# Optimization experiments

Measured on AMD Instinct MI355X. Metric: run time of the kernel, lower is better.

The kernel has to match this reference:

```python
import jax, jax.numpy as jnp
import numpy as np
from jax import lax

PART = 224   # PART_IMAGE_SIZE
PAD = 224    # PAD_SIZE
TOPN = 4
IOU_THRESH = 0.25
N_ANCHORS = 1614


def _conv(x, w, b, stride, pad):
    y = lax.conv_general_dilated(x, w, (stride, stride), [(pad, pad), (pad, pad)],
                                 dimension_numbers=('NCHW', 'OIHW', 'NCHW'))
    return y + b[None, :, None, None]


def _iou(box, boxes):
    # box [4], boxes [N,4] as (y0,x0,y1,x1)
    yy0 = jnp.maximum(box[0], boxes[:, 0]); xx0 = jnp.maximum(box[1], boxes[:, 1])
    yy1 = jnp.minimum(box[2], boxes[:, 2]); xx1 = jnp.minimum(box[3], boxes[:, 3])
    inter = jnp.clip(yy1 - yy0, 0.0) * jnp.clip(xx1 - xx0, 0.0)
    a = (box[2] - box[0]) * (box[3] - box[1])
    areas = (boxes[:, 2] - boxes[:, 0]) * (boxes[:, 3] - boxes[:, 1])
    return inter / (a + areas - inter)


def _nms(scores, boxes):
    # hard NMS keeping TOPN boxes; returns indices [TOPN]
    valid = jnp.ones(scores.shape, dtype=bool)
    idxs = []
    for _ in range(TOPN):
        i = jnp.argmax(jnp.where(valid, scores, -jnp.inf))
        idxs.append(i)
        valid = valid & (_iou(boxes[i], boxes) <= IOU_THRESH)
    return jnp.stack(idxs)


def _crop_resize(img, box):
    # img [3,Hp,Wp] padded image, box [4] float; bilinear, align_corners=True,
    # matching F.interpolate(x_pad[:, :, y0:y1, x0:x1], (PART, PART))
    Hp, Wp = img.shape[1], img.shape[2]
    def coords(c0, c1, L):
        t = jnp.arange(PART, dtype=img.dtype) / (PART - 1)
        c = c0 + (c1 - 1.0 - c0) * t          # absolute source coordinate
        cf = jnp.floor(c)
        lo = jnp.clip(cf.astype(jnp.int32), 0, L - 1)
        hi = jnp.clip(lo + 1, 0, L - 1)
        return lo, hi, c - cf
    yl, yh, wy = coords(box[0], box[2], Hp)
    xl, xh, wx = coords(box[1], box[3], Wp)
    g = lambda yi, xi: img[:, yi[:, None], xi[None, :]]   # [3,PART,PART]
    return ((1 - wy)[:, None] * ((1 - wx) * g(yl, xl) + wx * g(yl, xh))
            + wy[:, None] * ((1 - wx) * g(yh, xl) + wx * g(yh, xh)))


def setup_inputs() -> dict:
    key = jax.random.key(0)
    ks = jax.random.split(key, 20)
    x = jax.random.uniform(ks[0], (16, 3, 448, 448), dtype=jnp.float32)
    rpn_feature = jax.random.normal(ks[1], (16, 2048, 14, 14), dtype=jnp.float32)
    # valid boxes inside the padded 896x896 image
    y0 = jax.random.randint(ks[2], (N_ANCHORS,), 0, 560)
    x0 = jax.random.randint(ks[3], (N_ANCHORS,), 0, 560)
    h = jax.random.randint(ks[4], (N_ANCHORS,), 32, 336)
    w = jax.random.randint(ks[5], (N_ANCHORS,), 32, 336)
    anchors = jnp.stack([y0, x0, jnp.minimum(y0 + h, 896), jnp.minimum(x0 + w, 896)], axis=1).astype(jnp.int32)
    s = 0.02
    inp = {
        'x': x, 'rpn_feature': rpn_feature, 'anchors': anchors,
        'w_down1': jax.random.normal(ks[6], (128, 2048, 3, 3), jnp.float32) * s,
        'b_down1': jnp.zeros((128,), jnp.float32),
        'w_down2': jax.random.normal(ks[7], (128, 128, 3, 3), jnp.float32) * s,
        'b_down2': jnp.zeros((128,), jnp.float32),
        'w_down3': jax.random.normal(ks[8], (128, 128, 3, 3), jnp.float32) * s,
        'b_down3': jnp.zeros((128,), jnp.float32),
        'w_tidy1': jax.random.normal(ks[9], (6, 128, 1, 1), jnp.float32) * s,
        'b_tidy1': jnp.zeros((6,), jnp.float32),
        'w_tidy2': jax.random.normal(ks[10], (6, 128, 1, 1), jnp.float32) * s,
        'b_tidy2': jnp.zeros((6,), jnp.float32),
        'w_tidy3': jax.random.normal(ks[11], (9, 128, 1, 1), jnp.float32) * s,
        'b_tidy3': jnp.zeros((9,), jnp.float32),
    }
    return inp


def reference(x, rpn_feature, anchors,
              w_down1, b_down1, w_down2, b_down2, w_down3, b_down3,
              w_tidy1, b_tidy1, w_tidy2, b_tidy2, w_tidy3, b_tidy3):
    B = x.shape[0]
    # ProposalNet
    d1 = jax.nn.relu(_conv(rpn_feature, w_down1, b_down1, 1, 1))   # [B,128,14,14]
    d2 = jax.nn.relu(_conv(d1, w_down2, b_down2, 2, 1))            # [B,128,7,7]
    d3 = jax.nn.relu(_conv(d2, w_down3, b_down3, 2, 1))            # [B,128,4,4]
    t1 = _conv(d1, w_tidy1, b_tidy1, 1, 0).reshape(B, -1)
    t2 = _conv(d2, w_tidy2, b_tidy2, 1, 0).reshape(B, -1)
    t3 = _conv(d3, w_tidy3, b_tidy3, 1, 0).reshape(B, -1)
    rpn_score = jnp.concatenate([t1, t2, t3], axis=1)              # [B, 1614]
    boxes = anchors.astype(x.dtype)                                # [N,4]
    top_n_index = jax.vmap(lambda s: _nms(s, boxes))(rpn_score)    # [B,TOPN]
    top_n_prob = jnp.take_along_axis(rpn_score, top_n_index, axis=1)
    x_pad = jnp.pad(x, ((0, 0), (0, 0), (PAD, PAD), (PAD, PAD)))   # [B,3,896,896]
    sel_boxes = boxes[top_n_index]                                 # [B,TOPN,4]
    part_imgs = jax.vmap(lambda img, bxs: jax.vmap(lambda b: _crop_resize(img, b))(bxs))(x_pad, sel_boxes)
    # part_imgs: [B,TOPN,3,PART,PART]
    return rpn_score, top_n_index, top_n_prob, part_imgs
```

## Files before the change

### kernel.cpp

```cpp
#include <hip/hip_runtime.h>
#include <hip/hip_bf16.h>

#define NB 16
#define NA 1614
#define NBP (NB * 196 * 128)

typedef __bf16 bf16x8 __attribute__((ext_vector_type(8)));
typedef float f32x4 __attribute__((ext_vector_type(4)));

__device__ __forceinline__ unsigned short f2bf(float v) {
  unsigned u = __float_as_uint(v);
  unsigned r = (u + 0x7FFFu + ((u >> 16) & 1u)) >> 16;
  return (unsigned short)r;
}
__device__ __forceinline__ float bf2f(unsigned short s) {
  return __uint_as_float(((unsigned)s) << 16);
}

__global__ __launch_bounds__(256)
void prep(const float* __restrict__ w, const float* __restrict__ in,
          unsigned short* __restrict__ wTh, unsigned short* __restrict__ wTl,
          unsigned short* __restrict__ aTh, unsigned short* __restrict__ aTl) {
  __shared__ float s[32 * 201];
  const int bid = blockIdx.x;
  if (bid < 1024) {
    const int chunk = bid & 63, b = bid >> 6;
    const float* src = in + ((size_t)b * 2048 + chunk * 32) * 196;
#pragma unroll
    for (int r = 0; r < 7; r++) {
      int e = threadIdx.x + 256 * r;
      if (e < 1568) {
        int ic = e / 49, f = e - ic * 49;
        float4 v = ((const float4*)(src + (size_t)ic * 196))[f];
        float* d = s + ic * 201 + f * 4;
        d[0] = v.x; d[1] = v.y; d[2] = v.z; d[3] = v.w;
      }
    }
    __syncthreads();
    unsigned short* oh = aTh + (size_t)bid * (196 * 32);
    unsigned short* ol = aTl + (size_t)bid * (196 * 32);
#pragma unroll
    for (int r = 0; r < 4; r++) {
      int e = threadIdx.x + 256 * r;
      if (e < 784) {
        int pos = e >> 2, part = e & 3;
        unsigned short hv[8], lv[8];
#pragma unroll
        for (int j = 0; j < 8; j++) {
          float v = s[(part * 8 + j) * 201 + pos];
          unsigned short h = f2bf(v);
          hv[j] = h;
          lv[j] = f2bf(v - bf2f(h));
        }
        ((uint4*)oh)[e] = *(uint4*)hv;
        ((uint4*)ol)[e] = *(uint4*)lv;
      }
    }
  } else {
    int e = (bid - 1024) * 256 + threadIdx.x;
    if (e < 9 * 128 * 2048) {
      int tap = e / (128 * 2048);
      int rem = e - tap * (128 * 2048);
      int oc = rem >> 11, ic = rem & 2047;
      int kcp = ic >> 7, ks = (ic >> 5) & 3, icq = (ic >> 3) & 3, j = ic & 7;
      size_t g2 = ((size_t)(kcp * 36 + tap * 4 + ks) << 12) + oc * 32 + icq * 8 + j;
      float v = w[((size_t)oc * 2048 + ic) * 9 + tap];
      unsigned short h = f2bf(v);
      wTh[g2] = h;
      wTl[g2] = f2bf(v - bf2f(h));
    }
  }
}

#define APL 1360
#define ABUF (4 * APL)

#define LOADB(H, L, T, K)                                                     \
  {                                                                           \
    const size_t o_ = ((size_t)(kc * 36 + (T) * 4 + (K)) << 12) + bln;        \
    const unsigned short* ph_ = wTh + o_;                                     \
    const unsigned short* pq_ = wTl + o_;                                     \
    H[0] = *(const bf16x8*)(ph_);                                             \
    H[1] = *(const bf16x8*)(ph_ + 512);                                       \
    L[0] = *(const bf16x8*)(pq_);                                             \
    L[1] = *(const bf16x8*)(pq_ + 512);                                       \
  }

#define STEP(IT, BUH, BUL, BNH, BNL)                                          \
  {                                                                           \
    const int it_ = (IT);                                                     \
    const int ks_ = it_ / 9, tap_ = it_ - ks_ * 9;                            \
    {             \
      const int ni_ = (it_ < 35) ? it_ + 1 : 35;                              \
      const int nk_ = ni_ / 9, nt_ = ni_ - nk_ * 9;                           \
      LOADB(BNH, BNL, nt_, nk_);                                              \
    }                                                                         \
    if (ks_ < 3) {        \
      if (tap_ == 3 || tap_ == 4) {                                           \
        int e_ = tid + 256 * (tap_ - 3);                                      \
        if (e_ < ne) {                                                        \
          int u_ = pos04 + e_;                                                \
          int pos_ = u_ >> 2, part_ = u_ & 3;                                 \
          int py_ = pos_ / 14, px_ = pos_ - py_ * 14;                         \
          int d_ = (((ks_ + 1) & 1) ? ABUF : 0) + part_ * APL                 \
                   + (py_ + 1 - rowoff) * 136 + (px_ + 1) * 8;                \
          *(uint4*)(sAh + d_) = sgh;                                          \
          *(uint4*)(sAl + d_) = sgl;                                          \
        }                                                                     \
      }                                                                       \
      if (tap_ == 2 || tap_ == 3) {                                           \
        const uint4* gh_ = (const uint4*)(aTh + ((size_t)(b * 64 + kc * 4 + ks_ + 1) * 196) * 32); \
        const uint4* gl_ = (const uint4*)(aTl + ((size_t)(b * 64 + kc * 4 + ks_ + 1) * 196) * 32); \
        int e_ = tid + 256 * (tap_ - 2);                                      \
        if (e_ < ne) { sgh = gh_[pos04 + e_]; sgl = gl_[pos04 + e_]; }        \
      }                                                                       \
    }                                                                         \
    const int t8_ = (tap_ / 3) * 136 + (tap_ - (tap_ / 3) * 3) * 8;           \
    const unsigned short* pah_ = sAh + (ks_ & 1) * ABUF + qoff + t8_;         \
    const unsigned short* pal_ = sAl + (ks_ & 1) * ABUF + qoff + t8_;         \
    bf16x8 afh[7], afl[7];                                                    \
    _Pragma("unroll") for (int mf = 0; mf < 7; mf++) {                        \
      afh[mf] = *(const bf16x8*)(pah_ + abase[mf]);                           \
      afl[mf] = *(const bf16x8*)(pal_ + abase[mf]);                           \
    }                                                                         \
    _Pragma("unroll") for (int mf = 0; mf < 7; mf++)                          \
      _Pragma("unroll") for (int nf = 0; nf < 2; nf++)                        \
        acc[mf][nf] = __builtin_amdgcn_mfma_f32_16x16x32_bf16(afh[mf], BUH[nf], acc[mf][nf], 0, 0, 0); \
    _Pragma("unroll") for (int mf = 0; mf < 7; mf++)                          \
      _Pragma("unroll") for (int nf = 0; nf < 2; nf++)                        \
        acc[mf][nf] = __builtin_amdgcn_mfma_f32_16x16x32_bf16(afl[mf], BUH[nf], acc[mf][nf], 0, 0, 0); \
    _Pragma("unroll") for (int mf = 0; mf < 7; mf++)                          \
      _Pragma("unroll") for (int nf = 0; nf < 2; nf++)                        \
        acc[mf][nf] = __builtin_amdgcn_mfma_f32_16x16x32_bf16(afh[mf], BUL[nf], acc[mf][nf], 0, 0, 0); \
    if (tap_ == 8) __syncthreads();                                           \
  }

__global__ __launch_bounds__(256, 2)
void conv1_mfma(const unsigned short* __restrict__ aTh, const unsigned short* __restrict__ aTl,
                const unsigned short* __restrict__ wTh, const unsigned short* __restrict__ wTl,
                float* __restrict__ p1) {
  const int bid = blockIdx.x;
  const int kc = bid & 15;
  const int b  = (bid >> 4) & 15;
  const int mh = bid >> 8;
  const int tid = threadIdx.x;
  const int wid = tid >> 6, lane = tid & 63;
  const int wn = wid;
  const int q = lane >> 4, ln = lane & 15;

  __shared__ unsigned short sAh[2 * ABUF];
  __shared__ unsigned short sAl[2 * ABUF];

  const int rowoff = 6 * mh;
  const int pos0 = mh ? 98 : 0;
  const int ne   = mh ? 392 : 504;
  const int pos04 = pos0 * 4;

  for (int e = tid; e < 2 * ABUF / 2; e += 256) {
    ((unsigned int*)sAh)[e] = 0u;
    ((unsigned int*)sAl)[e] = 0u;
  }

  int abase[7];
#pragma unroll
  for (int mf = 0; mf < 7; mf++) {
    int row = mh * 112 + mf * 16 + ln;
    int y = row / 14, x = row - y * 14;
    abase[mf] = (row < 196) ? ((y - rowoff) * 136 + x * 8) : 0;
  }
  const int qoff = q * APL;
  const int bln = (wn * 32 + ln) * 32 + q * 8;

  f32x4 acc[7][2];
#pragma unroll
  for (int mf = 0; mf < 7; mf++)
#pragma unroll
    for (int nf = 0; nf < 2; nf++) acc[mf][nf] = (f32x4){0.f, 0.f, 0.f, 0.f};

  uint4 sgh = {}, sgl = {};

  __syncthreads();

  {
    const uint4* gh = (const uint4*)(aTh + ((size_t)(b * 64 + kc * 4) * 196) * 32);
    const uint4* gl = (const uint4*)(aTl + ((size_t)(b * 64 + kc * 4) * 196) * 32);
#pragma unroll
    for (int r = 0; r < 2; r++) {
      int e = tid + 256 * r;
      if (e < ne) {
        int u = pos04 + e;
        int pos = u >> 2, part = u & 3;
        int py = pos / 14, px = pos - py * 14;
        int d = part * APL + (py + 1 - rowoff) * 136 + (px + 1) * 8;
        *(uint4*)(sAh + d) = gh[u];
        *(uint4*)(sAl + d) = gl[u];
      }
    }
  }
  bf16x8 b0h[2], b0l[2], b1h[2], b1l[2];
  LOADB(b0h, b0l, 0, 0);
  __syncthreads();

  for (int it = 0; it < 36; it += 2) {
    STEP(it,     b0h, b0l, b1h, b1l);
    STEP(it + 1, b1h, b1l, b0h, b0l);
  }

  float* pk = p1 + ((size_t)kc * NB + b) * 196 * 128;
#pragma unroll
  for (int mf = 0; mf < 7; mf++) {
    const int row0 = mh * 112 + mf * 16 + q * 4;
#pragma unroll
    for (int nf = 0; nf < 2; nf++) {
      const int oc = wn * 32 + nf * 16 + ln;
#pragma unroll
      for (int r = 0; r < 4; r++) {
        const int row = row0 + r;
        if (row < 196) pk[(size_t)row * 128 + oc] = acc[mf][nf][r];
      }
    }
  }
}

__global__ __launch_bounds__(256)
void conv1_finish_p(const float* __restrict__ p1, const float* __restrict__ bias,
                    float* __restrict__ d1) {
  __shared__ float s[28 * 132];
  const int bid = blockIdx.x;
  const int pt = bid % 7, b = bid / 7;
  const int tid = threadIdx.x;
#pragma unroll
  for (int r = 0; r < 4; r++) {
    int u = tid + 256 * r;
    if (u < 896) {
      int pos = u >> 5, oc4 = u & 31;
      const float* base = p1 + ((size_t)(b * 196 + pt * 28 + pos)) * 128 + oc4 * 4;
      float4 sum = ((const float4*)bias)[oc4];
#pragma unroll
      for (int k = 0; k < 16; k++) {
        float4 v = *(const float4*)(base + (size_t)k * NBP);
        sum.x += v.x; sum.y += v.y; sum.z += v.z; sum.w += v.w;
      }
      sum.x = fmaxf(sum.x, 0.f); sum.y = fmaxf(sum.y, 0.f);
      sum.z = fmaxf(sum.z, 0.f); sum.w = fmaxf(sum.w, 0.f);
      *(float4*)(s + pos * 132 + oc4 * 4) = sum;
    }
  }
  __syncthreads();
#pragma unroll
  for (int r = 0; r < 4; r++) {
    int u = tid + 256 * r;
    if (u < 896) {
      int oc = u / 7, f = u - oc * 7;
      float4 v;
      v.x = s[(f * 4 + 0) * 132 + oc];
      v.y = s[(f * 4 + 1) * 132 + oc];
      v.z = s[(f * 4 + 2) * 132 + oc];
      v.w = s[(f * 4 + 3) * 132 + oc];
      *(float4*)(d1 + ((size_t)b * 128 + oc) * 196 + pt * 28 + f * 4) = v;
    }
  }
}

__global__ void conv2_part(const float* __restrict__ d1, const float* __restrict__ w,
                           float* __restrict__ p2) {
  const int bid = blockIdx.x;
  const int kc = bid & 3, oct = (bid >> 2) & 3, b = bid >> 4;
  const int ic0 = kc * 32, oc0 = oct * 32;
  const int tid = threadIdx.x;
  const int ocl = tid >> 3, rw = tid & 7;

  __shared__ float s_in[32 * 320];
  __shared__ float s_w[32 * 324];

#pragma unroll
  for (int r = 0; r < 32; r++) {
    const int e = tid + 256 * r;
    const int ch = e >> 8, idx = e & 255;
    const int tr = idx >> 4, tc = idx & 15;
    const int iy = tr - 1, ix = tc - 1;
    float v = 0.f;
    if ((unsigned)iy < 14u && (unsigned)ix < 14u)
      v = d1[((size_t)b * 128 + ic0 + ch) * 196 + iy * 14 + ix];
    s_in[ch * 320 + tr * 20 + tc] = v;
  }
#pragma unroll
  for (int r = 0; r < 36; r++) {
    const int e = tid + 256 * r;
    const int oc = e / 288, rem = e - oc * 288;
    const int ch = rem / 9, tap = rem - ch * 9;
    s_w[ch * 324 + tap * 36 + oc] =
        w[(size_t)(oc0 + oc) * 1152 + (size_t)ic0 * 9 + rem];
  }
  __syncthreads();

  if (rw < 7) {
    float acc[7] = {};
    for (int ic = 0; ic < 32; ic++) {
      const float* wrow = s_w + ic * 324 + ocl;
      const float* irow = s_in + ic * 320;
#pragma unroll
      for (int ky = 0; ky < 3; ky++) {
        const float* r = irow + (2 * rw + ky) * 20;
        const float4 f0 = *(const float4*)(r);
        const float4 f1 = *(const float4*)(r + 4);
        const float4 f2 = *(const float4*)(r + 8);
        const float4 f3 = *(const float4*)(r + 12);
        const float ev[8] = {f0.x, f0.z, f1.x, f1.z, f2.x, f2.z, f3.x, f3.z};
        const float od[7] = {f0.y, f0.w, f1.y, f1.w, f2.y, f2.w, f3.y};
        const float w0 = wrow[(ky * 3 + 0) * 36];
        const float w1 = wrow[(ky * 3 + 1) * 36];
        const float w2 = wrow[(ky * 3 + 2) * 36];
#pragma unroll
        for (int x = 0; x < 7; x++)
          acc[x] = fmaf(w0, ev[x], fmaf(w1, od[x], fmaf(w2, ev[x + 1], acc[x])));
      }
    }
    float* po = p2 + (((size_t)kc * NB + b) * 128 + oc0 + ocl) * 49 + rw * 7;
#pragma unroll
    for (int x = 0; x < 7; x++) po[x] = acc[x];
  }
}

__global__ void conv2_finish(const float* __restrict__ p2, const float* __restrict__ bias,
                             float* __restrict__ d2) {
  const int i = blockIdx.x * 256 + threadIdx.x;
  if (i >= NB * 128 * 49) return;
  const int oc = (i / 49) & 127;
  float s = bias[oc];
#pragma unroll
  for (int k = 0; k < 4; k++) s += p2[(size_t)k * (NB * 128 * 49) + i];
  d2[i] = fmaxf(s, 0.f);
}

__global__ void conv3_part(const float* __restrict__ d2, const float* __restrict__ w,
                           float* __restrict__ p3) {
  const int bid = blockIdx.x;
  const int kc = bid & 1, oct = (bid >> 1) & 7, b = bid >> 4;
  const int ic0 = kc * 64, oc0 = oct * 16;
  const int tid = threadIdx.x;
  const int oc = tid >> 4, p = tid & 15;
  const int y = p >> 2, x = p & 3;

  __shared__ float s_in[64 * 108];
  __shared__ float s_w[64 * 144];

#pragma unroll
  for (int r = 0; r < 21; r++) {
    const int e = tid + 256 * r;
    if (e < 64 * 81) {
      const int ch = e / 81, idx = e - ch * 81;
      const int tr = idx / 9, tc = idx - tr * 9;
      const int iy = tr - 1, ix = tc - 1;
      float v = 0.f;
      if ((unsigned)iy < 7u && (unsigned)ix < 7u)
        v = d2[((size_t)b * 128 + ic0 + ch) * 49 + iy * 7 + ix];
      s_in[ch * 108 + tr * 12 + tc] = v;
    }
  }
#pragma unroll
  for (int r = 0; r < 36; r++) {
    const int e = tid + 256 * r;
    const int o = e / 576, rem = e - o * 576;
    const int ch = rem / 9, tap = rem - ch * 9;
    s_w[ch * 144 + tap * 16 + o] =
        w[(size_t)(oc0 + o) * 1152 + (size_t)ic0 * 9 + rem];
  }
  __syncthreads();

  float acc = 0.f;
  for (int ic = 0; ic < 64; ic++) {
    const float* wrow = s_w + ic * 144 + oc;
    const float* irow = s_in + ic * 108 + 2 * y * 12 + 2 * x;
#pragma unroll
    for (int ky = 0; ky < 3; ky++)
#pragma unroll
      for (int kx = 0; kx < 3; kx++)
        acc = fmaf(wrow[(ky * 3 + kx) * 16], irow[ky * 12 + kx], acc);
  }
  p3[(((size_t)kc * NB + b) * 128 + oc0 + oc) * 16 + p] = acc;
}

__global__ __launch_bounds__(256, 1)
void score_nms(const float* __restrict__ d1, const float* __restrict__ d2,
               const float* __restrict__ p3, const float* __restrict__ bd3,
               const float* __restrict__ w1, const float* __restrict__ b1,
               const float* __restrict__ w2, const float* __restrict__ b2,
               const float* __restrict__ w3, const float* __restrict__ b3,
               const int* __restrict__ anchors, float* __restrict__ score,
               float* __restrict__ out_idx, float* __restrict__ out_prob,
               float* __restrict__ sel) {
  __shared__ float s_in[32 * 200];
  __shared__ float s_w[21 * 128];
  __shared__ float s_b[21];
  __shared__ float s_sc[NA];
  __shared__ float s_bx[NA * 4];
  __shared__ float r_s[256];
  __shared__ int r_i[256];
  const int b = blockIdx.x, tid = threadIdx.x;

  for (int i = tid; i < 768; i += 256) s_w[i] = w1[i];
  for (int i = tid; i < 768; i += 256) s_w[768 + i] = w2[i];
  for (int i = tid; i < 1152; i += 256) s_w[1536 + i] = w3[i];
  if (tid < 21) s_b[tid] = (tid < 6) ? b1[tid] : (tid < 12) ? b2[tid - 6] : b3[tid - 12];
  for (int i = tid; i < NA; i += 256) {
    s_bx[i * 4 + 0] = (float)anchors[i * 4 + 0];
    s_bx[i * 4 + 1] = (float)anchors[i * 4 + 1];
    s_bx[i * 4 + 2] = (float)anchors[i * 4 + 2];
    s_bx[i * 4 + 3] = (float)anchors[i * 4 + 3];
  }

  float acc[5] = {0.f, 0.f, 0.f, 0.f, 0.f};
  for (int chunk = 0; chunk < 4; chunk++) {
    __syncthreads();
    const float* src = d1 + ((size_t)b * 128 + chunk * 32) * 196;
#pragma unroll
    for (int r = 0; r < 7; r++) {
      int e = tid + 256 * r;
      if (e < 1568) {
        int ic = e / 49, f = e - ic * 49;
        *(float4*)(s_in + ic * 200 + f * 4) = ((const float4*)(src + (size_t)ic * 196))[f];
      }
    }
    __syncthreads();
#pragma unroll
    for (int k = 0; k < 5; k++) {
      int j = tid + 256 * k;
      if (j < 1176) {
        int oc = j / 196, p = j - oc * 196;
        const float* wr = s_w + oc * 128 + chunk * 32;
        float s = acc[k];
#pragma unroll
        for (int ic = 0; ic < 32; ic++) s = fmaf(wr[ic], s_in[ic * 200 + p], s);
        acc[k] = s;
      }
    }
  }
#pragma unroll
  for (int k = 0; k < 5; k++) {
    int j = tid + 256 * k;
    if (j < 1176) {
      int oc = j / 196;
      float s = acc[k] + s_b[oc];
      s_sc[j] = s;
      score[b * NA + j] = s;
    }
  }

  __syncthreads();
  {
    const float* src = d2 + (size_t)b * 6272;
#pragma unroll
    for (int r = 0; r < 7; r++) {
      int e = tid + 256 * r;
      if (e < 1568) *(float4*)(s_in + e * 4) = ((const float4*)src)[e];
    }
  }
  __syncthreads();
#pragma unroll
  for (int k = 0; k < 2; k++) {
    int jj = tid + 256 * k;
    if (jj < 294) {
      int oc = jj / 49, p = jj - oc * 49;
      const float* wr = s_w + 768 + oc * 128;
      float s = s_b[6 + oc];
#pragma unroll 8
      for (int ic = 0; ic < 128; ic++) s = fmaf(wr[ic], s_in[ic * 49 + p], s);
      s_sc[1176 + jj] = s;
      score[b * NA + 1176 + jj] = s;
    }
  }

  __syncthreads();
  {
    const float4* s0 = (const float4*)(p3 + (size_t)b * 2048);
    const float4* s1 = (const float4*)(p3 + 32768 + (size_t)b * 2048);
#pragma unroll
    for (int r = 0; r < 2; r++) {
      int e = tid + 256 * r;
      if (e < 512) {
        float4 a = s0[e], c = s1[e];
        float bb = bd3[e >> 2];
        float4 v;
        v.x = fmaxf(a.x + c.x + bb, 0.f);
        v.y = fmaxf(a.y + c.y + bb, 0.f);
        v.z = fmaxf(a.z + c.z + bb, 0.f);
        v.w = fmaxf(a.w + c.w + bb, 0.f);
        *(float4*)(s_in + e * 4) = v;
      }
    }
  }
  __syncthreads();
  if (tid < 144) {
    int oc = tid >> 4, p = tid & 15;
    const float* wr = s_w + 1536 + oc * 128;
    float s = s_b[12 + oc];
#pragma unroll 8
    for (int ic = 0; ic < 128; ic++) s = fmaf(wr[ic], s_in[ic * 16 + p], s);
    s_sc[1470 + tid] = s;
    score[b * NA + 1470 + tid] = s;
  }
  __syncthreads();

  for (int t = 0; t < 4; t++) {
    float bs = -__builtin_inff();
    int bi = NA;
    for (int i = tid; i < NA; i += 256) {
      float s = s_sc[i];
      if (s > bs || (s == bs && i < bi)) { bs = s; bi = i; }
    }
    r_s[tid] = bs; r_i[tid] = bi;
    __syncthreads();
    for (int off = 128; off > 0; off >>= 1) {
      if (tid < off) {
        float s2 = r_s[tid + off]; int i2 = r_i[tid + off];
        if (s2 > r_s[tid] || (s2 == r_s[tid] && i2 < r_i[tid])) { r_s[tid] = s2; r_i[tid] = i2; }
      }
      __syncthreads();
    }
    const int idx = r_i[0];
    const float by0 = s_bx[idx * 4 + 0], bx0 = s_bx[idx * 4 + 1];
    const float by1 = s_bx[idx * 4 + 2], bx1 = s_bx[idx * 4 + 3];
    if (tid == 0) {
      out_idx[b * 4 + t] = (float)idx;
      out_prob[b * 4 + t] = s_sc[idx];
      sel[(b * 4 + t) * 4 + 0] = by0;
      sel[(b * 4 + t) * 4 + 1] = bx0;
      sel[(b * 4 + t) * 4 + 2] = by1;
      sel[(b * 4 + t) * 4 + 3] = bx1;
    }
    __syncthreads();
    const float a = (by1 - by0) * (bx1 - bx0);
    for (int i = tid; i < NA; i += 256) {
      float cy0 = s_bx[i * 4 + 0], cx0 = s_bx[i * 4 + 1];
      float cy1 = s_bx[i * 4 + 2], cx1 = s_bx[i * 4 + 3];
      float yy0 = fmaxf(by0, cy0), xx0 = fmaxf(bx0, cx0);
      float yy1 = fminf(by1, cy1), xx1 = fminf(bx1, cx1);
      float inter = fmaxf(yy1 - yy0, 0.f) * fmaxf(xx1 - xx0, 0.f);
      float ar = (cy1 - cy0) * (cx1 - cx0);
      float iou = inter / (a + ar - inter);
      if (iou > 0.25f) s_sc[i] = -__builtin_inff();
    }
    __syncthreads();
  }
}

__global__ void crop_kernel(const float* __restrict__ x, const float* __restrict__ sel,
                            float* __restrict__ out) {
  int i4 = blockIdx.x * 256 + threadIdx.x;
  const int total4 = NB * 4 * 3 * 224 * 56;
  if (i4 >= total4) return;
  int px0 = (i4 % 56) * 4;
  int t = i4 / 56;
  int py = t % 224; t /= 224;
  int ch = t % 3;  t /= 3;
  int n  = t % 4;
  int b  = t / 4;

  const float* bx = sel + (b * 4 + n) * 4;
  const float y0 = bx[0], x0 = bx[1], y1 = bx[2], x1 = bx[3];

  float ty = (float)py / 223.0f;
  float cy = y0 + (y1 - 1.0f - y0) * ty;
  float cyf = floorf(cy);
  int ylo = (int)cyf; ylo = ylo < 0 ? 0 : (ylo > 895 ? 895 : ylo);
  int yhi = ylo + 1 > 895 ? 895 : ylo + 1;
  float wy = cy - cyf;

  const float* img = x + ((size_t)b * 3 + ch) * 448 * 448;
  auto g = [&](int yy, int xx) -> float {
    yy -= 224; xx -= 224;
    if ((unsigned)yy < 448u && (unsigned)xx < 448u)
      return img[(size_t)yy * 448 + xx];
    return 0.f;
  };

  float4 res;
  float* rp = &res.x;
#pragma unroll
  for (int k = 0; k < 4; k++) {
    float tx = (float)(px0 + k) / 223.0f;
    float cx = x0 + (x1 - 1.0f - x0) * tx;
    float cxf = floorf(cx);
    int xlo = (int)cxf; xlo = xlo < 0 ? 0 : (xlo > 895 ? 895 : xlo);
    int xhi = xlo + 1 > 895 ? 895 : xlo + 1;
    float wx = cx - cxf;
    float v00 = g(ylo, xlo), v01 = g(ylo, xhi);
    float v10 = g(yhi, xlo), v11 = g(yhi, xhi);
    rp[k] = (1.f - wy) * ((1.f - wx) * v00 + wx * v01) +
            wy * ((1.f - wx) * v10 + wx * v11);
  }
  *(float4*)(out + (size_t)i4 * 4) = res;
}

extern "C" void kernel_launch(void* const* d_in, const int* in_sizes, int n_in,
                              void* d_out, int out_size, void* d_ws, size_t ws_size,
                              hipStream_t stream) {
  const float* x    = (const float*)d_in[0];
  const float* rpn  = (const float*)d_in[1];
  const int*   anc  = (const int*)d_in[2];
  const float* w_d1 = (const float*)d_in[3];
  const float* b_d1 = (const float*)d_in[4];
  const float* w_d2 = (const float*)d_in[5];
  const float* b_d2 = (const float*)d_in[6];
  const float* w_d3 = (const float*)d_in[7];
  const float* b_d3 = (const float*)d_in[8];
  const float* w_t1 = (const float*)d_in[9];
  const float* b_t1 = (const float*)d_in[10];
  const float* w_t2 = (const float*)d_in[11];
  const float* b_t2 = (const float*)d_in[12];
  const float* w_t3 = (const float*)d_in[13];
  const float* b_t3 = (const float*)d_in[14];

  float* out = (float*)d_out;
  float* ws = (float*)d_ws;

  float* d1  = ws;
  float* d2  = d1 + 401408;
  float* d3  = d2 + 100352;
  float* sel = d3 + 32768;
  float* p2  = sel + 256;
  float* p3  = p2 + 401408;
  unsigned short* wTh = (unsigned short*)(p3 + 65536);
  unsigned short* wTl = wTh + 2359296;
  unsigned short* aTh = wTl + 2359296;
  unsigned short* aTl = aTh + 6422528;

  float* score    = out;
  float* out_idx  = out + 25824;
  float* out_prob = out + 25888;
  float* parts    = out + 25952;
  float* p1       = parts;

  prep<<<dim3(10240), dim3(256), 0, stream>>>(w_d1, rpn, wTh, wTl, aTh, aTl);
  conv1_mfma<<<dim3(512), dim3(256), 0, stream>>>(aTh, aTl, wTh, wTl, p1);
  conv1_finish_p<<<dim3(112), dim3(256), 0, stream>>>(p1, b_d1, d1);
  conv2_part<<<dim3(256), dim3(256), 0, stream>>>(d1, w_d2, p2);
  conv2_finish<<<dim3(392), dim3(256), 0, stream>>>(p2, b_d2, d2);
  conv3_part<<<dim3(256), dim3(256), 0, stream>>>(d2, w_d3, p3);
  score_nms<<<dim3(16), dim3(256), 0, stream>>>(d1, d2, p3, b_d3, w_t1, b_t1, w_t2, b_t2,
                                                w_t3, b_t3, anc, score, out_idx, out_prob, sel);
  crop_kernel<<<dim3(9408), dim3(256), 0, stream>>>(x, sel, parts);
}
```

Measured before the change: 275.9 us.

## Tile weight transpose via LDS, split conv2 over input channels, fuse conv2 finish

The weight-conversion part of prep now has each block load a contiguous 32x288 float slab with float4 reads into shared memory, then scatter it. This replaces one uncoalesced stride-9 gather per element and cuts that part of the grid from 9216 to 256 blocks. conv2_part now gives every thread 4 output channels and a quarter of the input channels, with a shared-memory reduction at the end, instead of leaving a warp idle per 8 threads. The conv2_finish kernel is removed and its bias+ReLU+partial-sum reduction is recomputed inside conv3_part and score_nms. That saves one launch and the d2 round trip, but the reduction work is repeated and p2 is read several times.

```diff
diff --git a/kernel.cpp b/kernel.cpp
--- a/kernel.cpp
+++ b/kernel.cpp
@@ -4,6 +4,7 @@
 #define NB 16
 #define NA 1614
 #define NBP (NB * 196 * 128)
+#define NBP2 (NB * 128 * 49)
 
 typedef __bf16 bf16x8 __attribute__((ext_vector_type(8)));
 typedef float f32x4 __attribute__((ext_vector_type(4)));
@@ -21,7 +22,7 @@
 void prep(const float* __restrict__ w, const float* __restrict__ in,
           unsigned short* __restrict__ wTh, unsigned short* __restrict__ wTl,
           unsigned short* __restrict__ aTh, unsigned short* __restrict__ aTl) {
-  __shared__ float s[32 * 201];
+  __shared__ float sbuf[32 * 289];
   const int bid = blockIdx.x;
   if (bid < 1024) {
     const int chunk = bid & 63, b = bid >> 6;
@@ -32,7 +33,7 @@
       if (e < 1568) {
         int ic = e / 49, f = e - ic * 49;
         float4 v = ((const float4*)(src + (size_t)ic * 196))[f];
-        float* d = s + ic * 201 + f * 4;
+        float* d = sbuf + ic * 201 + f * 4;
         d[0] = v.x; d[1] = v.y; d[2] = v.z; d[3] = v.w;
       }
     }
@@ -47,7 +48,7 @@
         unsigned short hv[8], lv[8];
 #pragma unroll
         for (int j = 0; j < 8; j++) {
-          float v = s[(part * 8 + j) * 201 + pos];
+          float v = sbuf[(part * 8 + j) * 201 + pos];
           unsigned short h = f2bf(v);
           hv[j] = h;
           lv[j] = f2bf(v - bf2f(h));
@@ -57,15 +58,27 @@
       }
     }
   } else {
-    int e = (bid - 1024) * 256 + threadIdx.x;
-    if (e < 9 * 128 * 2048) {
-      int tap = e / (128 * 2048);
-      int rem = e - tap * (128 * 2048);
-      int oc = rem >> 11, ic = rem & 2047;
-      int kcp = ic >> 7, ks = (ic >> 5) & 3, icq = (ic >> 3) & 3, j = ic & 7;
-      size_t g2 = ((size_t)(kcp * 36 + tap * 4 + ks) << 12) + oc * 32 + icq * 8 + j;
-      float v = w[((size_t)oc * 2048 + ic) * 9 + tap];
+    const int bid2 = bid - 1024;
+    const int ocg = bid2 & 3, ks = (bid2 >> 2) & 3, kcp = bid2 >> 4;
+    const int oc0 = ocg * 32;
+    const int ic0 = kcp * 128 + ks * 32;
+#pragma unroll
+    for (int r = 0; r < 9; r++) {
+      int f = threadIdx.x + 256 * r;
+      int o = f / 72, rem4 = f - o * 72;
+      float4 v = *(const float4*)(w + ((size_t)(oc0 + o) * 2048 + ic0) * 9 + rem4 * 4);
+      float* d = sbuf + o * 289 + rem4 * 4;
+      d[0] = v.x; d[1] = v.y; d[2] = v.z; d[3] = v.w;
+    }
+    __syncthreads();
+#pragma unroll
+    for (int r = 0; r < 36; r++) {
+      int e = threadIdx.x + 256 * r;
+      int tap = e >> 10, rem = e & 1023;
+      int o = rem >> 5, ic = rem & 31;
+      float v = sbuf[o * 289 + ic * 9 + tap];
       unsigned short h = f2bf(v);
+      size_t g2 = ((size_t)(kcp * 36 + tap * 4 + ks) << 12) + oc0 * 32 + rem;
       wTh[g2] = h;
       wTl[g2] = f2bf(v - bf2f(h));
     }
@@ -268,7 +281,9 @@
   const int kc = bid & 3, oct = (bid >> 2) & 3, b = bid >> 4;
   const int ic0 = kc * 32, oc0 = oct * 32;
   const int tid = threadIdx.x;
-  const int ocl = tid >> 3, rw = tid & 7;
+  const int icg = tid >> 6;
+  const int ocq = (tid >> 3) & 7;
+  const int rw  = tid & 7;
 
   __shared__ float s_in[32 * 320];
   __shared__ float s_w[32 * 324];
@@ -294,11 +309,17 @@
   }
   __syncthreads();
 
+  float acc[4][7];
+#pragma unroll
+  for (int oc = 0; oc < 4; oc++)
+#pragma unroll
+    for (int x = 0; x < 7; x++) acc[oc][x] = 0.f;
+
   if (rw < 7) {
-    float acc[7] = {};
-    for (int ic = 0; ic < 32; ic++) {
-      const float* wrow = s_w + ic * 324 + ocl;
-      const float* irow = s_in + ic * 320;
+    for (int ic = 0; ic < 8; ic++) {
+      const int ci = icg * 8 + ic;
+      const float* irow = s_in + ci * 320;
+      const float* wq = s_w + ci * 324 + ocq * 4;
 #pragma unroll
       for (int ky = 0; ky < 3; ky++) {
         const float* r = irow + (2 * rw + ky) * 20;
@@ -308,33 +329,51 @@
         const float4 f3 = *(const float4*)(r + 12);
         const float ev[8] = {f0.x, f0.z, f1.x, f1.z, f2.x, f2.z, f3.x, f3.z};
         const float od[7] = {f0.y, f0.w, f1.y, f1.w, f2.y, f2.w, f3.y};
-        const float w0 = wrow[(ky * 3 + 0) * 36];
-        const float w1 = wrow[(ky * 3 + 1) * 36];
-        const float w2 = wrow[(ky * 3 + 2) * 36];
-#pragma unroll
-        for (int x = 0; x < 7; x++)
-          acc[x] = fmaf(w0, ev[x], fmaf(w1, od[x], fmaf(w2, ev[x + 1], acc[x])));
-      }
-    }
-    float* po = p2 + (((size_t)kc * NB + b) * 128 + oc0 + ocl) * 49 + rw * 7;
-#pragma unroll
-    for (int x = 0; x < 7; x++) po[x] = acc[x];
-  }
-}
-
-__global__ void conv2_finish(const float* __restrict__ p2, const float* __restrict__ bias,
-                             float* __restrict__ d2) {
-  const int i = blockIdx.x * 256 + threadIdx.x;
-  if (i >= NB * 128 * 49) return;
-  const int oc = (i / 49) & 127;
-  float s = bias[oc];
-#pragma unroll
-  for (int k = 0; k < 4; k++) s += p2[(size_t)k * (NB * 128 * 49) + i];
-  d2[i] = fmaxf(s, 0.f);
-}
-
-__global__ void conv3_part(const float* __restrict__ d2, const float* __restrict__ w,
-                           float* __restrict__ p3) {
+        const float4 w0 = *(const float4*)(wq + (ky * 3 + 0) * 36);
+        const float4 w1 = *(const float4*)(wq + (ky * 3 + 1) * 36);
+        const float4 w2 = *(const float4*)(wq + (ky * 3 + 2) * 36);
+        const float w0a[4] = {w0.x, w0.y, w0.z, w0.w};
+        const float w1a[4] = {w1.x, w1.y, w1.z, w1.w};
+        const float w2a[4] = {w2.x, w2.y, w2.z, w2.w};
+#pragma unroll
+        for (int oc = 0; oc < 4; oc++) {
+          const float a0 = w0a[oc], a1 = w1a[oc], a2 = w2a[oc];
+#pragma unroll
+          for (int x = 0; x < 7; x++)
+            acc[oc][x] = fmaf(a0, ev[x], fmaf(a1, od[x], fmaf(a2, ev[x + 1], acc[oc][x])));
+        }
+      }
+    }
+  }
+  __syncthreads();
+
+  if (icg > 0 && rw < 7) {
+    float* dst = s_w + ((icg - 1) * 56 + ocq * 7 + rw) * 28;
+#pragma unroll
+    for (int oc = 0; oc < 4; oc++)
+#pragma unroll
+      for (int x = 0; x < 7; x++) dst[oc * 7 + x] = acc[oc][x];
+  }
+  __syncthreads();
+  if (icg == 0 && rw < 7) {
+#pragma unroll
+    for (int g = 0; g < 3; g++) {
+      const float* src = s_w + (g * 56 + ocq * 7 + rw) * 28;
+#pragma unroll
+      for (int oc = 0; oc < 4; oc++)
+#pragma unroll
+        for (int x = 0; x < 7; x++) acc[oc][x] += src[oc * 7 + x];
+    }
+    float* po = p2 + (((size_t)kc * NB + b) * 128 + oc0 + ocq * 4) * 49 + rw * 7;
+#pragma unroll
+    for (int oc = 0; oc < 4; oc++)
+#pragma unroll
+      for (int x = 0; x < 7; x++) po[oc * 49 + x] = acc[oc][x];
+  }
+}
+
+__global__ void conv3_part(const float* __restrict__ p2, const float* __restrict__ bd2,
+                           const float* __restrict__ w, float* __restrict__ p3) {
   const int bid = blockIdx.x;
   const int kc = bid & 1, oct = (bid >> 1) & 7, b = bid >> 4;
   const int ic0 = kc * 64, oc0 = oct * 16;
@@ -353,8 +392,14 @@
       const int tr = idx / 9, tc = idx - tr * 9;
       const int iy = tr - 1, ix = tc - 1;
       float v = 0.f;
-      if ((unsigned)iy < 7u && (unsigned)ix < 7u)
-        v = d2[((size_t)b * 128 + ic0 + ch) * 49 + iy * 7 + ix];
+      if ((unsigned)iy < 7u && (unsigned)ix < 7u) {
+        const size_t ii = ((size_t)b * 128 + ic0 + ch) * 49 + iy * 7 + ix;
+        v = bd2[ic0 + ch] + p2[ii];
+        v += p2[(size_t)NBP2 + ii];
+        v += p2[(size_t)2 * NBP2 + ii];
+        v += p2[(size_t)3 * NBP2 + ii];
+        v = fmaxf(v, 0.f);
+      }
       s_in[ch * 108 + tr * 12 + tc] = v;
     }
   }
@@ -382,7 +427,8 @@
 }
 
 __global__ __launch_bounds__(256, 1)
-void score_nms(const float* __restrict__ d1, const float* __restrict__ d2,
+void score_nms(const float* __restrict__ d1,
+               const float* __restrict__ p2, const float* __restrict__ bd2,
                const float* __restrict__ p3, const float* __restrict__ bd3,
                const float* __restrict__ w1, const float* __restrict__ b1,
                const float* __restrict__ w2, const float* __restrict__ b2,
@@ -449,11 +495,30 @@
 
   __syncthreads();
   {
-    const float* src = d2 + (size_t)b * 6272;
+    const size_t base = (size_t)b * 6272;
 #pragma unroll
     for (int r = 0; r < 7; r++) {
       int e = tid + 256 * r;
-      if (e < 1568) *(float4*)(s_in + e * 4) = ((const float4*)src)[e];
+      if (e < 1568) {
+        const float4 v0 = *(const float4*)(p2 + base + e * 4);
+        const float4 v1 = *(const float4*)(p2 + (size_t)NBP2 + base + e * 4);
+        const float4 v2 = *(const float4*)(p2 + (size_t)2 * NBP2 + base + e * 4);
+        const float4 v3 = *(const float4*)(p2 + (size_t)3 * NBP2 + base + e * 4);
+        const float s0[4] = {v0.x, v0.y, v0.z, v0.w};
+        const float s1[4] = {v1.x, v1.y, v1.z, v1.w};
+        const float s2[4] = {v2.x, v2.y, v2.z, v2.w};
+        const float s3[4] = {v3.x, v3.y, v3.z, v3.w};
+        float o[4];
+#pragma unroll
+        for (int k = 0; k < 4; k++) {
+          const int oc = (e * 4 + k) / 49;
+          float s = bd2[oc] + s0[k];
+          s += s1[k]; s += s2[k]; s += s3[k];
+          o[k] = fmaxf(s, 0.f);
+        }
+        float4 vv; vv.x = o[0]; vv.y = o[1]; vv.z = o[2]; vv.w = o[3];
+        *(float4*)(s_in + e * 4) = vv;
+      }
     }
   }
   __syncthreads();
@@ -632,13 +697,12 @@
   float* parts    = out + 25952;
   float* p1       = parts;
 
-  prep<<<dim3(10240), dim3(256), 0, stream>>>(w_d1, rpn, wTh, wTl, aTh, aTl);
+  prep<<<dim3(1280), dim3(256), 0, stream>>>(w_d1, rpn, wTh, wTl, aTh, aTl);
   conv1_mfma<<<dim3(512), dim3(256), 0, stream>>>(aTh, aTl, wTh, wTl, p1);
   conv1_finish_p<<<dim3(112), dim3(256), 0, stream>>>(p1, b_d1, d1);
   conv2_part<<<dim3(256), dim3(256), 0, stream>>>(d1, w_d2, p2);
-  conv2_finish<<<dim3(392), dim3(256), 0, stream>>>(p2, b_d2, d2);
-  conv3_part<<<dim3(256), dim3(256), 0, stream>>>(d2, w_d3, p3);
-  score_nms<<<dim3(16), dim3(256), 0, stream>>>(d1, d2, p3, b_d3, w_t1, b_t1, w_t2, b_t2,
+  conv3_part<<<dim3(256), dim3(256), 0, stream>>>(p2, b_d2, w_d3, p3);
+  score_nms<<<dim3(16), dim3(256), 0, stream>>>(d1, p2, b_d2, p3, b_d3, w_t1, b_t1, w_t2, b_t2,
                                                 w_t3, b_t3, anc, score, out_idx, out_prob, sel);
   crop_kernel<<<dim3(9408), dim3(256), 0, stream>>>(x, sel, parts);
 }
```

Measured after the change: 277.5 us. Within noise of the previous version (+0.6%).
